# Kernel tuning notes

Hardware: AMD Instinct MI355X
Metric: run time of the kernel (lower is better)

Reference implementation:

```python
import jax, jax.numpy as jnp
import numpy as np

NUM_DIM = 2
N, P, Q, C = 2048, 2048, 64, 2

def _mlp(x, layers, activate_final):
    n = len(layers)
    for i, (w, b) in enumerate(layers):
        x = x @ w + b
        if i < n - 1 or activate_final:
            x = jnp.tanh(x)
    return x

def setup_inputs() -> dict:
    key = jax.random.key(0)
    ks = jax.random.split(key, 24)
    s = 0.3  # param scale for numerical sanity
    return {
        "phase_coords": jax.random.normal(ks[0], (N, 2 * NUM_DIM), jnp.float32),
        "boundary_coords": jax.random.normal(ks[1], (N, 2 * NUM_DIM), jnp.float32),
        "coeff_position": jax.random.normal(ks[2], (P, NUM_DIM), jnp.float32),
        "coeff_values": jax.random.uniform(ks[3], (P, C), jnp.float32),
        "scattering_kernel_coords": jax.random.normal(ks[4], (Q, NUM_DIM), jnp.float32),
        "scattering_kernel": jax.random.uniform(ks[5], (Q,), jnp.float32),
        "velocity_weights": jax.random.uniform(ks[6], (Q,), jnp.float32) / Q,
        "attn_w1": s * jax.random.normal(ks[7], (6, 32), jnp.float32),
        "attn_b1": jnp.zeros((32,), jnp.float32),
        "attn_w2": s * jax.random.normal(ks[8], (32, 32), jnp.float32),
        "attn_b2": jnp.zeros((32,), jnp.float32),
        "attn_w3": s * jax.random.normal(ks[9], (32, 1), jnp.float32),
        "attn_b3": jnp.zeros((1,), jnp.float32),
        "green_w1": s * jax.random.normal(ks[10], (4 * NUM_DIM + C, 64), jnp.float32),
        "green_b1": jnp.zeros((64,), jnp.float32),
        "green_w2": s * jax.random.normal(ks[11], (64, 64), jnp.float32),
        "green_b2": jnp.zeros((64,), jnp.float32),
        "green_w3": s * jax.random.normal(ks[12], (64, 64), jnp.float32),
        "green_b3": jnp.zeros((64,), jnp.float32),
        "res_w": s * jax.random.normal(ks[13], (64, 64), jnp.float32),
        "res_b": jnp.zeros((64,), jnp.float32),
        "final_w": s * jax.random.normal(ks[14], (64, 1), jnp.float32),
        "final_b": jnp.zeros((1,), jnp.float32),
    }

def reference(phase_coords, boundary_coords, coeff_position, coeff_values,
              scattering_kernel_coords, scattering_kernel, velocity_weights,
              attn_w1, attn_b1, attn_w2, attn_b2, attn_w3, attn_b3,
              green_w1, green_b1, green_w2, green_b2, green_w3, green_b3,
              res_w, res_b, final_w, final_b):
    attn_layers = [(attn_w1, attn_b1), (attn_w2, attn_b2), (attn_w3, attn_b3)]
    green_layers = [(green_w1, green_b1), (green_w2, green_b2), (green_w3, green_b3)]

    x, v = phase_coords[:, :NUM_DIM], phase_coords[:, NUM_DIM:]     # (N,2),(N,2)
    xp, vp = boundary_coords[:, :NUM_DIM], boundary_coords[:, NUM_DIM:]

    # --- CoefficientNet: MLP attention logits + geometric mask + softmax over P ---
    ang = v / jnp.sqrt(jnp.sum(v**2, -1, keepdims=True) + 1e-16)     # (N,2)
    rel = x[:, None, :] - coeff_position[None, :, :]                 # (N,P,2)
    dist = jnp.sqrt(jnp.sum(rel**2, -1) + 1e-16)                     # (N,P)
    pos_loc = jnp.einsum('npd,nd->np', rel, ang)                     # (N,P)
    ang_loc = pos_loc / (dist + 1e-8)
    frames = jnp.stack([ang_loc, pos_loc], -1)                       # (N,P,2)
    coords = jnp.concatenate([x, v], -1)                             # (N,4)
    qk = jnp.concatenate(
        [jnp.broadcast_to(coords[:, None, :], (coords.shape[0], frames.shape[1], coords.shape[1])), frames], -1)  # (N,P,6)
    logits = _mlp(qk, attn_layers, False)[..., 0]                    # (N,P)
    logits = jnp.where(pos_loc > 0, logits, -1e30)
    aw = jax.nn.softmax(logits, axis=-1)
    coeff = jnp.exp(-(aw @ coeff_values))                            # (N,C)

    # --- GreenFunctionBlock (coefficients only depend on (x,v)) ---
    g0 = jnp.exp(_mlp(jnp.concatenate([x, v, xp, vp, coeff], -1), green_layers, True))  # (N,64)

    # --- res block depth=1: quadrature over velocity_prime (argnum=3) ---
    w_quad = (1.0 - scattering_kernel) * velocity_weights            # (Q,)
    Nn = x.shape[0]; Qq = scattering_kernel_coords.shape[0]
    base = jnp.concatenate([x, v, xp], -1)                           # (N,6)
    inp_q = jnp.concatenate([
        jnp.broadcast_to(base[:, None, :], (Nn, Qq, base.shape[1])),
        jnp.broadcast_to(scattering_kernel_coords[None, :, :], (Nn, Qq, NUM_DIM)),
        jnp.broadcast_to(coeff[:, None, :], (Nn, Qq, coeff.shape[1])),
    ], -1)                                                           # (N,Q,10)
    gq = jnp.exp(_mlp(inp_q, green_layers, True))                    # (N,Q,64)
    quad = jnp.einsum('nqh,q->nh', gq, w_quad)                       # (N,64)
    res = jnp.tanh(quad @ res_w + res_b)                             # widths[-1:], activate_final
    out = g0 + res
    return out @ final_w + final_b                                   # (N,1)
```

## Files before the change

kernel.cpp:

```cpp
#include <hip/hip_runtime.h>

#define NN 2048
#define PP 2048
#define QQ 64
#define GR_ROWS 4
#define GR_SLOTS 80
#define GR_MT 5

typedef __attribute__((ext_vector_type(8))) short short8;
typedef __attribute__((ext_vector_type(4))) float f32x4;
typedef __attribute__((ext_vector_type(4))) unsigned u32x4;

union V4 { u32x4 u; short8 s; };

#if __has_builtin(__builtin_amdgcn_exp2f)
#define EXP2(x) __builtin_amdgcn_exp2f(x)
#else
#define EXP2(x) exp2f(x)
#endif

__device__ __forceinline__ float fast_rcp(float x) { return __builtin_amdgcn_rcpf(x); }

__device__ __forceinline__ float fast_tanh(float x) {
    float t = EXP2(x * 2.885390082f);
    return 1.0f - 2.0f * __builtin_amdgcn_rcpf(t + 1.0f);
}

__device__ __forceinline__ unsigned cvt_pk_bf16(float lo, float hi) {
    unsigned r;
    asm("v_cvt_pk_bf16_f32 %0, %1, %2" : "=v"(r) : "v"(lo), "v"(hi));
    return r;
}
__device__ __forceinline__ unsigned short bf16_bits(float f) {
    unsigned u = __builtin_bit_cast(unsigned, f);
    u += 0x7FFFu + ((u >> 16) & 1u);
    return (unsigned short)(u >> 16);
}

__global__ __launch_bounds__(512) void attn_kernel(
    const float* __restrict__ pc, const float* __restrict__ cp,
    const float* __restrict__ cv,
    const float* __restrict__ w1, const float* __restrict__ b1,
    const float* __restrict__ w2, const float* __restrict__ b2,
    const float* __restrict__ w3, const float* __restrict__ b3,
    float* __restrict__ coeff_out)
{
    __shared__ float2 sap[8][272];
    __shared__ unsigned short sidx[8][272];
    __shared__ float sred[24];

    const int t = threadIdx.x;
    const int w = t >> 6, lane = t & 63;
    const int c15 = lane & 15, kg = lane >> 4;
    const int k0 = kg * 8;
    const int n  = blockIdx.x;
    const int p0 = w * 256;

    const float b3v = b3[0];
    const float x0 = pc[n*4+0], x1 = pc[n*4+1];
    const float v0 = pc[n*4+2], v1 = pc[n*4+3];
    const float rinv = __builtin_amdgcn_rsqf(v0*v0 + v1*v1 + 1e-16f);
    const float a0 = v0 * rinv, a1 = v1 * rinv;

    int cnt = 0;
    #pragma unroll
    for (int i = 0; i < 4; ++i) {
        const int p = p0 + i*64 + lane;
        const float2 cpp = ((const float2*)cp)[p];
        const float r0 = x0 - cpp.x;
        const float r1 = x1 - cpp.y;
        const float pos = fmaf(r0, a0, r1*a1);
        const bool f = pos > 0.0f;
        const unsigned long long mask = __ballot(f);
        if (f) {
            const int idx = cnt + __popcll(mask & ((1ull << lane) - 1ull));
            const float dist = sqrtf(r0*r0 + r1*r1 + 1e-16f);
            const float angl = pos * fast_rcp(dist + 1e-8f);
            sap[w][idx]  = make_float2(angl, pos);
            sidx[w][idx] = (unsigned short)p;
        }
        cnt += __popcll(mask);
    }
    if (lane < 16) {
        sap[w][cnt + lane]  = make_float2(0.0f, 0.0f);
        sidx[w][cnt + lane] = 0;
    }

    union BF { short8 s8; unsigned u[4]; } B0, B1;
    #pragma unroll
    for (int j2 = 0; j2 < 4; ++j2) {
        const int ka = k0 + 2*j2, kb = ka + 1;
        B0.u[j2] = cvt_pk_bf16(w2[ka*32 + c15],      w2[kb*32 + c15]);
        B1.u[j2] = cvt_pk_bf16(w2[ka*32 + c15 + 16], w2[kb*32 + c15 + 16]);
    }
    float b2a[4], b2b[4], w3a[4], w3b[4];
    #pragma unroll
    for (int r = 0; r < 4; ++r) {
        b2a[r] = b2[kg*4 + r];      b2b[r] = b2[16 + kg*4 + r];
        w3a[r] = w3[kg*4 + r];      w3b[r] = w3[16 + kg*4 + r];
    }
    float cfrag[8], w1a[8], w1b[8];
    #pragma unroll
    for (int j = 0; j < 8; ++j) {
        const int k = k0 + j;
        float c = b1[k];
        c = fmaf(x0, w1[0*32+k], c);
        c = fmaf(x1, w1[1*32+k], c);
        c = fmaf(v0, w1[2*32+k], c);
        c = fmaf(v1, w1[3*32+k], c);
        cfrag[j] = c;
        w1a[j] = w1[4*32+k];
        w1b[j] = w1[5*32+k];
    }
    float sw3 = 0.0f;
    #pragma unroll
    for (int j = 0; j < 32; ++j) sw3 += fabsf(w3[j]);
    const float Lb = fabsf(b3v) + sw3;
    const float C_E = (b3v - Lb) * 1.44269504f;

    float s = 0.0f, q0 = 0.0f, q1 = 0.0f;
    const int nt = (cnt + 15) >> 4;
    #pragma unroll 2
    for (int tile = 0; tile < nt; ++tile) {
        const int li = tile*16 + c15;
        const float2 ap = sap[w][li];
        const float angl = ap.x, pos = ap.y;

        float pre[8], h[8];
        #pragma unroll
        for (int j = 0; j < 8; ++j)
            pre[j] = fmaf(angl, w1a[j], fmaf(pos, w1b[j], cfrag[j]));
        #pragma unroll
        for (int j = 0; j < 8; ++j) h[j] = fast_tanh(pre[j]);

        union AF { short8 s8; unsigned u[4]; } H;
        #pragma unroll
        for (int j2 = 0; j2 < 4; ++j2)
            H.u[j2] = cvt_pk_bf16(h[2*j2], h[2*j2+1]);

        f32x4 acca = {b2a[0], b2a[1], b2a[2], b2a[3]};
        f32x4 accb = {b2b[0], b2b[1], b2b[2], b2b[3]};
        acca = __builtin_amdgcn_mfma_f32_16x16x32_bf16(B0.s8, H.s8, acca, 0, 0, 0);
        accb = __builtin_amdgcn_mfma_f32_16x16x32_bf16(B1.s8, H.s8, accb, 0, 0, 0);

        float lg = 0.0f;
        #pragma unroll
        for (int r = 0; r < 4; ++r) {
            lg = fmaf(fast_tanh(acca[r]), w3a[r], lg);
            lg = fmaf(fast_tanh(accb[r]), w3b[r], lg);
        }
        lg += __shfl_xor(lg, 16);
        lg += __shfl_xor(lg, 32);

        const bool val = (kg == 0) && (li < cnt);
        const int pidx = (int)sidx[w][li];
        const float2 cvv = ((const float2*)cv)[pidx];
        const float e = val ? EXP2(fmaf(lg, 1.44269504f, C_E)) : 0.0f;
        s += e;
        q0 = fmaf(e, cvv.x, q0);
        q1 = fmaf(e, cvv.y, q1);
    }

    #pragma unroll
    for (int off = 1; off < 64; off <<= 1) {
        s  += __shfl_xor(s, off);
        q0 += __shfl_xor(q0, off);
        q1 += __shfl_xor(q1, off);
    }
    if (lane == 0) {
        sred[w*3 + 0] = s;
        sred[w*3 + 1] = q0;
        sred[w*3 + 2] = q1;
    }
    __syncthreads();
    if (t == 0) {
        float S = 0.0f, Q0 = 0.0f, Q1 = 0.0f;
        #pragma unroll
        for (int i = 0; i < 8; ++i) {
            S  += sred[i*3 + 0];
            Q0 += sred[i*3 + 1];
            Q1 += sred[i*3 + 2];
        }
        if (!(S > 0.0f)) {
            S = (float)PP; Q0 = 0.0f; Q1 = 0.0f;
            for (int p = 0; p < PP; ++p) { Q0 += cv[2*p]; Q1 += cv[2*p+1]; }
        }
        const float invS = fast_rcp(S);
        coeff_out[n*2+0] = __expf(-Q0 * invS);
        coeff_out[n*2+1] = __expf(-Q1 * invS);
    }
}

__global__ __launch_bounds__(256) void green_kernel(
    const float* __restrict__ pc,  const float* __restrict__ bc,
    const float* __restrict__ skc, const float* __restrict__ sk,
    const float* __restrict__ vw,
    const float* __restrict__ gw1, const float* __restrict__ gb1,
    const float* __restrict__ gw2, const float* __restrict__ gb2,
    const float* __restrict__ gw3, const float* __restrict__ gb3,
    const float* __restrict__ rw,  const float* __restrict__ rb,
    const float* __restrict__ fw,  const float* __restrict__ fb,
    const float* __restrict__ coeff,
    float* __restrict__ out)
{
    __shared__ unsigned short sinA[GR_ROWS*GR_SLOTS*16];
    __shared__ unsigned short shb[4][16*64];
    __shared__ float swq[GR_SLOTS];
    __shared__ float sg0[4][64];
    __shared__ float squad[4][64];

    const int t = threadIdx.x;
    const int w = t >> 6, lane = t & 63;
    const int c15 = lane & 15, kg = lane >> 4;
    const int n0 = blockIdx.x * GR_ROWS;

    V4 Bw1[4], Bw2[2][4], Bw3[2][4];
    #pragma unroll
    for (int nt = 0; nt < 4; ++nt) {
        const int col = c15 + nt*16;
        #pragma unroll
        for (int j2 = 0; j2 < 4; ++j2) {
            const int ka = kg*8 + 2*j2, kb = ka + 1;
            const float va = (ka < 10) ? gw1[ka*64 + col] : 0.0f;
            const float vb = (kb < 10) ? gw1[kb*64 + col] : 0.0f;
            Bw1[nt].u[j2] = cvt_pk_bf16(va, vb);
        }
        #pragma unroll
        for (int kt = 0; kt < 2; ++kt) {
            #pragma unroll
            for (int j2 = 0; j2 < 4; ++j2) {
                const int ka = kt*32 + kg*8 + 2*j2, kb = ka + 1;
                Bw2[kt][nt].u[j2] = cvt_pk_bf16(gw2[ka*64 + col], gw2[kb*64 + col]);
                Bw3[kt][nt].u[j2] = cvt_pk_bf16(gw3[ka*64 + col], gw3[kb*64 + col]);
            }
        }
    }
    float b1c[4], b2c[4], b3c[4];
    #pragma unroll
    for (int nt = 0; nt < 4; ++nt) {
        b1c[nt] = gb1[c15 + nt*16];
        b2c[nt] = gb2[c15 + nt*16];
        b3c[nt] = gb3[c15 + nt*16];
    }

    for (int row = t; row < GR_ROWS*GR_SLOTS; row += 256) {
        const int nl = row / GR_SLOTS;
        const int s  = row - nl*GR_SLOTS;
        const int n  = n0 + nl;
        u32x4 lo = {0u,0u,0u,0u}, hi = {0u,0u,0u,0u};
        if (s <= 64) {
            const float X0 = pc[n*4+0], X1 = pc[n*4+1];
            const float V0 = pc[n*4+2], V1 = pc[n*4+3];
            const float XP0 = bc[n*4+0], XP1 = bc[n*4+1];
            float I6, I7;
            if (s == 64) { I6 = bc[n*4+2]; I7 = bc[n*4+3]; }
            else         { I6 = skc[s*2+0]; I7 = skc[s*2+1]; }
            const float C0 = coeff[n*2+0], C1 = coeff[n*2+1];
            lo[0] = cvt_pk_bf16(X0, X1);
            lo[1] = cvt_pk_bf16(V0, V1);
            lo[2] = cvt_pk_bf16(XP0, XP1);
            lo[3] = cvt_pk_bf16(I6, I7);
            hi[0] = cvt_pk_bf16(C0, C1);
        }
        ((u32x4*)sinA)[row*2 + 0] = lo;
        ((u32x4*)sinA)[row*2 + 1] = hi;
    }
    if (t < GR_SLOTS)
        swq[t] = (t < QQ) ? (1.0f - sk[t]) * vw[t] : 0.0f;
    __syncthreads();

    unsigned short* hb = &shb[w][0];
    float qacc[4] = {0.f, 0.f, 0.f, 0.f};

    #pragma unroll 1
    for (int T = 0; T < GR_MT; ++T) {
        const int rm = w*GR_SLOTS + T*16 + c15;
        V4 A1; A1.u = (u32x4){0u,0u,0u,0u};
        if (kg < 2) A1.u = ((u32x4*)sinA)[rm*2 + kg];

        f32x4 acc1[4];
        #pragma unroll
        for (int nt = 0; nt < 4; ++nt) {
            f32x4 a = {b1c[nt], b1c[nt], b1c[nt], b1c[nt]};
            acc1[nt] = __builtin_amdgcn_mfma_f32_16x16x32_bf16(A1.s, Bw1[nt].s, a, 0, 0, 0);
        }
        #pragma unroll
        for (int nt = 0; nt < 4; ++nt) {
            #pragma unroll
            for (int r = 0; r < 4; ++r) {
                const int rl = kg*4 + r;
                hb[rl*64 + ((c15 + nt*16) ^ ((rl&7)<<3))] = bf16_bits(fast_tanh(acc1[nt][r]));
            }
        }
        V4 A2[2];
        #pragma unroll
        for (int kt = 0; kt < 2; ++kt)
            A2[kt].u = ((u32x4*)hb)[(c15*64 + ((kt*32 + kg*8) ^ ((c15&7)<<3))) >> 3];
        f32x4 acc2[4];
        #pragma unroll
        for (int nt = 0; nt < 4; ++nt) {
            f32x4 a = {b2c[nt], b2c[nt], b2c[nt], b2c[nt]};
            a = __builtin_amdgcn_mfma_f32_16x16x32_bf16(A2[0].s, Bw2[0][nt].s, a, 0, 0, 0);
            acc2[nt] = __builtin_amdgcn_mfma_f32_16x16x32_bf16(A2[1].s, Bw2[1][nt].s, a, 0, 0, 0);
        }
        #pragma unroll
        for (int nt = 0; nt < 4; ++nt) {
            #pragma unroll
            for (int r = 0; r < 4; ++r) {
                const int rl = kg*4 + r;
                hb[rl*64 + ((c15 + nt*16) ^ ((rl&7)<<3))] = bf16_bits(fast_tanh(acc2[nt][r]));
            }
        }
        V4 A3[2];
        #pragma unroll
        for (int kt = 0; kt < 2; ++kt)
            A3[kt].u = ((u32x4*)hb)[(c15*64 + ((kt*32 + kg*8) ^ ((c15&7)<<3))) >> 3];
        f32x4 acc3[4];
        #pragma unroll
        for (int nt = 0; nt < 4; ++nt) {
            f32x4 a = {b3c[nt], b3c[nt], b3c[nt], b3c[nt]};
            a = __builtin_amdgcn_mfma_f32_16x16x32_bf16(A3[0].s, Bw3[0][nt].s, a, 0, 0, 0);
            acc3[nt] = __builtin_amdgcn_mfma_f32_16x16x32_bf16(A3[1].s, Bw3[1][nt].s, a, 0, 0, 0);
        }
        #pragma unroll
        for (int r = 0; r < 4; ++r) {
            const int s = T*16 + kg*4 + r;
            const float wq = swq[s];
            #pragma unroll
            for (int nt = 0; nt < 4; ++nt) {
                const float g = __expf(fast_tanh(acc3[nt][r]));
                qacc[nt] = fmaf(wq, g, qacc[nt]);
                if (T == GR_MT-1 && kg == 0 && r == 0) sg0[w][c15 + nt*16] = g;
            }
        }
    }

    #pragma unroll
    for (int nt = 0; nt < 4; ++nt) {
        qacc[nt] += __shfl_xor(qacc[nt], 16);
        qacc[nt] += __shfl_xor(qacc[nt], 32);
    }
    if (kg == 0) {
        #pragma unroll
        for (int nt = 0; nt < 4; ++nt) squad[w][c15 + nt*16] = qacc[nt];
    }

    const int k = lane;
    float r0a = rb[k], r1a = 0.f, r2a = 0.f, r3a = 0.f;
    #pragma unroll
    for (int j = 0; j < 64; j += 4) {
        const float4 qd = *(const float4*)&squad[w][j];
        r0a = fmaf(qd.x, rw[(j+0)*64 + k], r0a);
        r1a = fmaf(qd.y, rw[(j+1)*64 + k], r1a);
        r2a = fmaf(qd.z, rw[(j+2)*64 + k], r2a);
        r3a = fmaf(qd.w, rw[(j+3)*64 + k], r3a);
    }
    const float resv = fast_tanh((r0a + r1a) + (r2a + r3a));
    float term = (sg0[w][k] + resv) * fw[k];
    #pragma unroll
    for (int off = 32; off; off >>= 1) term += __shfl_xor(term, off);
    if (lane == 0) out[n0 + w] = term + fb[0];
}

extern "C" void kernel_launch(void* const* d_in, const int* in_sizes, int n_in,
                              void* d_out, int out_size, void* d_ws, size_t ws_size,
                              hipStream_t stream) {
    const float* pc  = (const float*)d_in[0];
    const float* bc  = (const float*)d_in[1];
    const float* cp  = (const float*)d_in[2];
    const float* cv  = (const float*)d_in[3];
    const float* skc = (const float*)d_in[4];
    const float* sk  = (const float*)d_in[5];
    const float* vw  = (const float*)d_in[6];
    const float* aw1 = (const float*)d_in[7];
    const float* ab1 = (const float*)d_in[8];
    const float* aw2 = (const float*)d_in[9];
    const float* ab2 = (const float*)d_in[10];
    const float* aw3 = (const float*)d_in[11];
    const float* ab3 = (const float*)d_in[12];
    const float* gw1 = (const float*)d_in[13];
    const float* gb1 = (const float*)d_in[14];
    const float* gw2 = (const float*)d_in[15];
    const float* gb2 = (const float*)d_in[16];
    const float* gw3 = (const float*)d_in[17];
    const float* gb3 = (const float*)d_in[18];
    const float* rw  = (const float*)d_in[19];
    const float* rb  = (const float*)d_in[20];
    const float* fw  = (const float*)d_in[21];
    const float* fb  = (const float*)d_in[22];

    float* coeff = (float*)d_ws;
    float* outp  = (float*)d_out;

    attn_kernel<<<NN, 512, 0, stream>>>(pc, cp, cv, aw1, ab1, aw2, ab2, aw3, ab3, coeff);
    green_kernel<<<NN/GR_ROWS, 256, 0, stream>>>(pc, bc, skc, sk, vw,
                                                 gw1, gb1, gw2, gb2, gw3, gb3,
                                                 rw, rb, fw, fb, coeff, outp);
}
```

Before: 80.24 us.

## Process two query rows per attention block and pack angle/pos as bf16 in LDS

The attention kernel now handles two query points per 512-thread block, with four waves per point each scanning 512 candidates instead of eight waves each scanning 256. This halves the block count and the per-block fixed costs such as weight loading and the final reduction. The stored angle/position pair is packed into one bf16x2 word to fit the larger per-wave LDS buffers. That rounds the MLP inputs earlier than before and may slightly change accuracy. Fewer waves cooperate per point, so load imbalance across waves may grow.

```diff
diff --git a/kernel.cpp b/kernel.cpp
--- a/kernel.cpp
+++ b/kernel.cpp
@@ -35,6 +35,12 @@
     unsigned u = __builtin_bit_cast(unsigned, f);
     u += 0x7FFFu + ((u >> 16) & 1u);
     return (unsigned short)(u >> 16);
+}
+__device__ __forceinline__ float bf16_lo(unsigned pk) {
+    return __builtin_bit_cast(float, pk << 16);
+}
+__device__ __forceinline__ float bf16_hi(unsigned pk) {
+    return __builtin_bit_cast(float, pk & 0xFFFF0000u);
 }
 
 __global__ __launch_bounds__(512) void attn_kernel(
@@ -45,16 +51,16 @@
     const float* __restrict__ w3, const float* __restrict__ b3,
     float* __restrict__ coeff_out)
 {
-    __shared__ float2 sap[8][272];
-    __shared__ unsigned short sidx[8][272];
+    __shared__ unsigned sap[8][528];
+    __shared__ unsigned short sidx[8][528];
     __shared__ float sred[24];
 
     const int t = threadIdx.x;
     const int w = t >> 6, lane = t & 63;
     const int c15 = lane & 15, kg = lane >> 4;
     const int k0 = kg * 8;
-    const int n  = blockIdx.x;
-    const int p0 = w * 256;
+    const int n  = blockIdx.x * 2 + (w >> 2);
+    const int p0 = (w & 3) * 512;
 
     const float b3v = b3[0];
     const float x0 = pc[n*4+0], x1 = pc[n*4+1];
@@ -64,7 +70,7 @@
 
     int cnt = 0;
     #pragma unroll
-    for (int i = 0; i < 4; ++i) {
+    for (int i = 0; i < 8; ++i) {
         const int p = p0 + i*64 + lane;
         const float2 cpp = ((const float2*)cp)[p];
         const float r0 = x0 - cpp.x;
@@ -76,13 +82,13 @@
             const int idx = cnt + __popcll(mask & ((1ull << lane) - 1ull));
             const float dist = sqrtf(r0*r0 + r1*r1 + 1e-16f);
             const float angl = pos * fast_rcp(dist + 1e-8f);
-            sap[w][idx]  = make_float2(angl, pos);
+            sap[w][idx]  = cvt_pk_bf16(angl, pos);
             sidx[w][idx] = (unsigned short)p;
         }
         cnt += __popcll(mask);
     }
     if (lane < 16) {
-        sap[w][cnt + lane]  = make_float2(0.0f, 0.0f);
+        sap[w][cnt + lane]  = 0u;
         sidx[w][cnt + lane] = 0;
     }
 
@@ -123,8 +129,8 @@
     #pragma unroll 2
     for (int tile = 0; tile < nt; ++tile) {
         const int li = tile*16 + c15;
-        const float2 ap = sap[w][li];
-        const float angl = ap.x, pos = ap.y;
+        const unsigned pk = sap[w][li];
+        const float angl = bf16_lo(pk), pos = bf16_hi(pk);
 
         float pre[8], h[8];
         #pragma unroll
@@ -173,13 +179,13 @@
         sred[w*3 + 2] = q1;
     }
     __syncthreads();
-    if (t == 0) {
+    if (lane == 0 && (w == 0 || w == 4)) {
         float S = 0.0f, Q0 = 0.0f, Q1 = 0.0f;
         #pragma unroll
-        for (int i = 0; i < 8; ++i) {
-            S  += sred[i*3 + 0];
-            Q0 += sred[i*3 + 1];
-            Q1 += sred[i*3 + 2];
+        for (int i = 0; i < 4; ++i) {
+            S  += sred[(w + i)*3 + 0];
+            Q0 += sred[(w + i)*3 + 1];
+            Q1 += sred[(w + i)*3 + 2];
         }
         if (!(S > 0.0f)) {
             S = (float)PP; Q0 = 0.0f; Q1 = 0.0f;
@@ -392,7 +398,7 @@
     float* coeff = (float*)d_ws;
     float* outp  = (float*)d_out;
 
-    attn_kernel<<<NN, 512, 0, stream>>>(pc, cp, cv, aw1, ab1, aw2, ab2, aw3, ab3, coeff);
+    attn_kernel<<<NN/2, 512, 0, stream>>>(pc, cp, cv, aw1, ab1, aw2, ab2, aw3, ab3, coeff);
     green_kernel<<<NN/GR_ROWS, 256, 0, stream>>>(pc, bc, skc, sk, vw,
                                                  gw1, gb1, gw2, gb2, gw3, gb3,
                                                  rw, rb, fw, fb, coeff, outp);
```

Measured after the change: 83.35 us. 3.9% more time.

## Fuse attention and Green-function kernels into one per-row kernel

Applied to the files above, without the earlier changes.

Merges the attention-coefficient kernel and the Green-function MLP/quadrature kernel into a single 512-thread kernel, one block per row. Coefficients pass through shared memory instead of a global workspace, which removes the second launch and the global round trip. The 80 quadrature slots are split across 5 waves, and a final wave does the residual layer and output. The cost is that each block reloads and converts the Green MLP weights to bf16 for a single row instead of amortising them over 4 rows. Three of the eight waves also sit idle during the Green phase, and shared-memory use per block rises.

```diff
diff --git a/kernel.cpp b/kernel.cpp
--- a/kernel.cpp
+++ b/kernel.cpp
@@ -3,9 +3,6 @@
 #define NN 2048
 #define PP 2048
 #define QQ 64
-#define GR_ROWS 4
-#define GR_SLOTS 80
-#define GR_MT 5
 
 typedef __attribute__((ext_vector_type(8))) short short8;
 typedef __attribute__((ext_vector_type(4))) float f32x4;
@@ -37,17 +34,31 @@
     return (unsigned short)(u >> 16);
 }
 
-__global__ __launch_bounds__(512) void attn_kernel(
-    const float* __restrict__ pc, const float* __restrict__ cp,
-    const float* __restrict__ cv,
+__global__ __launch_bounds__(512) void fused_kernel(
+    const float* __restrict__ pc,  const float* __restrict__ bc,
+    const float* __restrict__ cp,  const float* __restrict__ cv,
+    const float* __restrict__ skc, const float* __restrict__ sk,
+    const float* __restrict__ vw,
     const float* __restrict__ w1, const float* __restrict__ b1,
     const float* __restrict__ w2, const float* __restrict__ b2,
     const float* __restrict__ w3, const float* __restrict__ b3,
-    float* __restrict__ coeff_out)
+    const float* __restrict__ gw1, const float* __restrict__ gb1,
+    const float* __restrict__ gw2, const float* __restrict__ gb2,
+    const float* __restrict__ gw3, const float* __restrict__ gb3,
+    const float* __restrict__ rw,  const float* __restrict__ rb,
+    const float* __restrict__ fw,  const float* __restrict__ fb,
+    float* __restrict__ out)
 {
     __shared__ float2 sap[8][272];
     __shared__ unsigned short sidx[8][272];
     __shared__ float sred[24];
+    __shared__ float scoef[2];
+    __shared__ unsigned short sinA[80*16];
+    __shared__ unsigned short shb[5][16*64];
+    __shared__ float swq[80];
+    __shared__ float sq[5][64];
+    __shared__ float sg0[64];
+    __shared__ float squadL[64];
 
     const int t = threadIdx.x;
     const int w = t >> 6, lane = t & 63;
@@ -119,9 +130,9 @@
     const float C_E = (b3v - Lb) * 1.44269504f;
 
     float s = 0.0f, q0 = 0.0f, q1 = 0.0f;
-    const int nt = (cnt + 15) >> 4;
+    const int ntl = (cnt + 15) >> 4;
     #pragma unroll 2
-    for (int tile = 0; tile < nt; ++tile) {
+    for (int tile = 0; tile < ntl; ++tile) {
         const int li = tile*16 + c15;
         const float2 ap = sap[w][li];
         const float angl = ap.x, pos = ap.y;
@@ -173,6 +184,7 @@
         sred[w*3 + 2] = q1;
     }
     __syncthreads();
+
     if (t == 0) {
         float S = 0.0f, Q0 = 0.0f, Q1 = 0.0f;
         #pragma unroll
@@ -186,180 +198,149 @@
             for (int p = 0; p < PP; ++p) { Q0 += cv[2*p]; Q1 += cv[2*p+1]; }
         }
         const float invS = fast_rcp(S);
-        coeff_out[n*2+0] = __expf(-Q0 * invS);
-        coeff_out[n*2+1] = __expf(-Q1 * invS);
-    }
-}
-
-__global__ __launch_bounds__(256) void green_kernel(
-    const float* __restrict__ pc,  const float* __restrict__ bc,
-    const float* __restrict__ skc, const float* __restrict__ sk,
-    const float* __restrict__ vw,
-    const float* __restrict__ gw1, const float* __restrict__ gb1,
-    const float* __restrict__ gw2, const float* __restrict__ gb2,
-    const float* __restrict__ gw3, const float* __restrict__ gb3,
-    const float* __restrict__ rw,  const float* __restrict__ rb,
-    const float* __restrict__ fw,  const float* __restrict__ fb,
-    const float* __restrict__ coeff,
-    float* __restrict__ out)
-{
-    __shared__ unsigned short sinA[GR_ROWS*GR_SLOTS*16];
-    __shared__ unsigned short shb[4][16*64];
-    __shared__ float swq[GR_SLOTS];
-    __shared__ float sg0[4][64];
-    __shared__ float squad[4][64];
-
-    const int t = threadIdx.x;
-    const int w = t >> 6, lane = t & 63;
-    const int c15 = lane & 15, kg = lane >> 4;
-    const int n0 = blockIdx.x * GR_ROWS;
-
-    V4 Bw1[4], Bw2[2][4], Bw3[2][4];
-    #pragma unroll
-    for (int nt = 0; nt < 4; ++nt) {
-        const int col = c15 + nt*16;
-        #pragma unroll
-        for (int j2 = 0; j2 < 4; ++j2) {
-            const int ka = kg*8 + 2*j2, kb = ka + 1;
-            const float va = (ka < 10) ? gw1[ka*64 + col] : 0.0f;
-            const float vb = (kb < 10) ? gw1[kb*64 + col] : 0.0f;
-            Bw1[nt].u[j2] = cvt_pk_bf16(va, vb);
-        }
-        #pragma unroll
-        for (int kt = 0; kt < 2; ++kt) {
-            #pragma unroll
-            for (int j2 = 0; j2 < 4; ++j2) {
-                const int ka = kt*32 + kg*8 + 2*j2, kb = ka + 1;
-                Bw2[kt][nt].u[j2] = cvt_pk_bf16(gw2[ka*64 + col], gw2[kb*64 + col]);
-                Bw3[kt][nt].u[j2] = cvt_pk_bf16(gw3[ka*64 + col], gw3[kb*64 + col]);
-            }
-        }
-    }
-    float b1c[4], b2c[4], b3c[4];
-    #pragma unroll
-    for (int nt = 0; nt < 4; ++nt) {
-        b1c[nt] = gb1[c15 + nt*16];
-        b2c[nt] = gb2[c15 + nt*16];
-        b3c[nt] = gb3[c15 + nt*16];
-    }
-
-    for (int row = t; row < GR_ROWS*GR_SLOTS; row += 256) {
-        const int nl = row / GR_SLOTS;
-        const int s  = row - nl*GR_SLOTS;
-        const int n  = n0 + nl;
+        scoef[0] = __expf(-Q0 * invS);
+        scoef[1] = __expf(-Q1 * invS);
+    }
+    __syncthreads();
+
+    if (t < 80) {
+        const int slot = t;
         u32x4 lo = {0u,0u,0u,0u}, hi = {0u,0u,0u,0u};
-        if (s <= 64) {
-            const float X0 = pc[n*4+0], X1 = pc[n*4+1];
-            const float V0 = pc[n*4+2], V1 = pc[n*4+3];
+        if (slot <= 64) {
             const float XP0 = bc[n*4+0], XP1 = bc[n*4+1];
             float I6, I7;
-            if (s == 64) { I6 = bc[n*4+2]; I7 = bc[n*4+3]; }
-            else         { I6 = skc[s*2+0]; I7 = skc[s*2+1]; }
-            const float C0 = coeff[n*2+0], C1 = coeff[n*2+1];
-            lo[0] = cvt_pk_bf16(X0, X1);
-            lo[1] = cvt_pk_bf16(V0, V1);
+            if (slot == 64) { I6 = bc[n*4+2]; I7 = bc[n*4+3]; }
+            else            { I6 = skc[slot*2+0]; I7 = skc[slot*2+1]; }
+            lo[0] = cvt_pk_bf16(x0, x1);
+            lo[1] = cvt_pk_bf16(v0, v1);
             lo[2] = cvt_pk_bf16(XP0, XP1);
             lo[3] = cvt_pk_bf16(I6, I7);
-            hi[0] = cvt_pk_bf16(C0, C1);
-        }
-        ((u32x4*)sinA)[row*2 + 0] = lo;
-        ((u32x4*)sinA)[row*2 + 1] = hi;
-    }
-    if (t < GR_SLOTS)
-        swq[t] = (t < QQ) ? (1.0f - sk[t]) * vw[t] : 0.0f;
+            hi[0] = cvt_pk_bf16(scoef[0], scoef[1]);
+        }
+        ((u32x4*)sinA)[slot*2 + 0] = lo;
+        ((u32x4*)sinA)[slot*2 + 1] = hi;
+        swq[slot] = (slot < QQ) ? (1.0f - sk[slot]) * vw[slot] : 0.0f;
+    }
     __syncthreads();
 
-    unsigned short* hb = &shb[w][0];
-    float qacc[4] = {0.f, 0.f, 0.f, 0.f};
-
-    #pragma unroll 1
-    for (int T = 0; T < GR_MT; ++T) {
-        const int rm = w*GR_SLOTS + T*16 + c15;
+    if (w < 5) {
+        const int rm = w*16 + c15;
         V4 A1; A1.u = (u32x4){0u,0u,0u,0u};
-        if (kg < 2) A1.u = ((u32x4*)sinA)[rm*2 + kg];
-
-        f32x4 acc1[4];
-        #pragma unroll
-        for (int nt = 0; nt < 4; ++nt) {
-            f32x4 a = {b1c[nt], b1c[nt], b1c[nt], b1c[nt]};
-            acc1[nt] = __builtin_amdgcn_mfma_f32_16x16x32_bf16(A1.s, Bw1[nt].s, a, 0, 0, 0);
+        if (kg < 2) A1.u = ((const u32x4*)sinA)[rm*2 + kg];
+        unsigned short* hb = &shb[w][0];
+
+        f32x4 acc[4];
+        #pragma unroll
+        for (int nt = 0; nt < 4; ++nt) {
+            const int col = c15 + nt*16;
+            V4 B;
+            #pragma unroll
+            for (int j2 = 0; j2 < 4; ++j2) {
+                const int ka = kg*8 + 2*j2, kb = ka + 1;
+                const float va = (ka < 10) ? gw1[ka*64 + col] : 0.0f;
+                const float vb = (kb < 10) ? gw1[kb*64 + col] : 0.0f;
+                B.u[j2] = cvt_pk_bf16(va, vb);
+            }
+            const float bb = gb1[col];
+            f32x4 a = {bb, bb, bb, bb};
+            acc[nt] = __builtin_amdgcn_mfma_f32_16x16x32_bf16(A1.s, B.s, a, 0, 0, 0);
         }
         #pragma unroll
         for (int nt = 0; nt < 4; ++nt) {
             #pragma unroll
             for (int r = 0; r < 4; ++r) {
                 const int rl = kg*4 + r;
-                hb[rl*64 + ((c15 + nt*16) ^ ((rl&7)<<3))] = bf16_bits(fast_tanh(acc1[nt][r]));
+                hb[rl*64 + ((c15 + nt*16) ^ ((rl&7)<<3))] = bf16_bits(fast_tanh(acc[nt][r]));
             }
         }
         V4 A2[2];
         #pragma unroll
         for (int kt = 0; kt < 2; ++kt)
             A2[kt].u = ((u32x4*)hb)[(c15*64 + ((kt*32 + kg*8) ^ ((c15&7)<<3))) >> 3];
-        f32x4 acc2[4];
-        #pragma unroll
-        for (int nt = 0; nt < 4; ++nt) {
-            f32x4 a = {b2c[nt], b2c[nt], b2c[nt], b2c[nt]};
-            a = __builtin_amdgcn_mfma_f32_16x16x32_bf16(A2[0].s, Bw2[0][nt].s, a, 0, 0, 0);
-            acc2[nt] = __builtin_amdgcn_mfma_f32_16x16x32_bf16(A2[1].s, Bw2[1][nt].s, a, 0, 0, 0);
+        #pragma unroll
+        for (int nt = 0; nt < 4; ++nt) {
+            const int col = c15 + nt*16;
+            V4 Ba, Bb;
+            #pragma unroll
+            for (int j2 = 0; j2 < 4; ++j2) {
+                const int ka = kg*8 + 2*j2, kb = ka + 1;
+                Ba.u[j2] = cvt_pk_bf16(gw2[ka*64 + col],        gw2[kb*64 + col]);
+                Bb.u[j2] = cvt_pk_bf16(gw2[(32+ka)*64 + col],   gw2[(32+kb)*64 + col]);
+            }
+            const float bb = gb2[col];
+            f32x4 a = {bb, bb, bb, bb};
+            a = __builtin_amdgcn_mfma_f32_16x16x32_bf16(A2[0].s, Ba.s, a, 0, 0, 0);
+            acc[nt] = __builtin_amdgcn_mfma_f32_16x16x32_bf16(A2[1].s, Bb.s, a, 0, 0, 0);
         }
         #pragma unroll
         for (int nt = 0; nt < 4; ++nt) {
             #pragma unroll
             for (int r = 0; r < 4; ++r) {
                 const int rl = kg*4 + r;
-                hb[rl*64 + ((c15 + nt*16) ^ ((rl&7)<<3))] = bf16_bits(fast_tanh(acc2[nt][r]));
+                hb[rl*64 + ((c15 + nt*16) ^ ((rl&7)<<3))] = bf16_bits(fast_tanh(acc[nt][r]));
             }
         }
         V4 A3[2];
         #pragma unroll
         for (int kt = 0; kt < 2; ++kt)
             A3[kt].u = ((u32x4*)hb)[(c15*64 + ((kt*32 + kg*8) ^ ((c15&7)<<3))) >> 3];
-        f32x4 acc3[4];
-        #pragma unroll
-        for (int nt = 0; nt < 4; ++nt) {
-            f32x4 a = {b3c[nt], b3c[nt], b3c[nt], b3c[nt]};
-            a = __builtin_amdgcn_mfma_f32_16x16x32_bf16(A3[0].s, Bw3[0][nt].s, a, 0, 0, 0);
-            acc3[nt] = __builtin_amdgcn_mfma_f32_16x16x32_bf16(A3[1].s, Bw3[1][nt].s, a, 0, 0, 0);
-        }
+        #pragma unroll
+        for (int nt = 0; nt < 4; ++nt) {
+            const int col = c15 + nt*16;
+            V4 Ba, Bb;
+            #pragma unroll
+            for (int j2 = 0; j2 < 4; ++j2) {
+                const int ka = kg*8 + 2*j2, kb = ka + 1;
+                Ba.u[j2] = cvt_pk_bf16(gw3[ka*64 + col],        gw3[kb*64 + col]);
+                Bb.u[j2] = cvt_pk_bf16(gw3[(32+ka)*64 + col],   gw3[(32+kb)*64 + col]);
+            }
+            const float bb = gb3[col];
+            f32x4 a = {bb, bb, bb, bb};
+            a = __builtin_amdgcn_mfma_f32_16x16x32_bf16(A3[0].s, Ba.s, a, 0, 0, 0);
+            acc[nt] = __builtin_amdgcn_mfma_f32_16x16x32_bf16(A3[1].s, Bb.s, a, 0, 0, 0);
+        }
+        float qpart[4] = {0.f, 0.f, 0.f, 0.f};
         #pragma unroll
         for (int r = 0; r < 4; ++r) {
-            const int s = T*16 + kg*4 + r;
-            const float wq = swq[s];
+            const int slot = w*16 + kg*4 + r;
+            const float wq = swq[slot];
             #pragma unroll
             for (int nt = 0; nt < 4; ++nt) {
-                const float g = __expf(fast_tanh(acc3[nt][r]));
-                qacc[nt] = fmaf(wq, g, qacc[nt]);
-                if (T == GR_MT-1 && kg == 0 && r == 0) sg0[w][c15 + nt*16] = g;
-            }
-        }
-    }
-
-    #pragma unroll
-    for (int nt = 0; nt < 4; ++nt) {
-        qacc[nt] += __shfl_xor(qacc[nt], 16);
-        qacc[nt] += __shfl_xor(qacc[nt], 32);
-    }
-    if (kg == 0) {
-        #pragma unroll
-        for (int nt = 0; nt < 4; ++nt) squad[w][c15 + nt*16] = qacc[nt];
-    }
-
-    const int k = lane;
-    float r0a = rb[k], r1a = 0.f, r2a = 0.f, r3a = 0.f;
-    #pragma unroll
-    for (int j = 0; j < 64; j += 4) {
-        const float4 qd = *(const float4*)&squad[w][j];
-        r0a = fmaf(qd.x, rw[(j+0)*64 + k], r0a);
-        r1a = fmaf(qd.y, rw[(j+1)*64 + k], r1a);
-        r2a = fmaf(qd.z, rw[(j+2)*64 + k], r2a);
-        r3a = fmaf(qd.w, rw[(j+3)*64 + k], r3a);
-    }
-    const float resv = fast_tanh((r0a + r1a) + (r2a + r3a));
-    float term = (sg0[w][k] + resv) * fw[k];
-    #pragma unroll
-    for (int off = 32; off; off >>= 1) term += __shfl_xor(term, off);
-    if (lane == 0) out[n0 + w] = term + fb[0];
+                const float g = __expf(fast_tanh(acc[nt][r]));
+                qpart[nt] = fmaf(wq, g, qpart[nt]);
+                if (w == 4 && kg == 0 && r == 0) sg0[c15 + nt*16] = g;
+            }
+        }
+        #pragma unroll
+        for (int nt = 0; nt < 4; ++nt) {
+            qpart[nt] += __shfl_xor(qpart[nt], 16);
+            qpart[nt] += __shfl_xor(qpart[nt], 32);
+        }
+        if (kg == 0) {
+            #pragma unroll
+            for (int nt = 0; nt < 4; ++nt) sq[w][c15 + nt*16] = qpart[nt];
+        }
+    }
+    __syncthreads();
+
+    if (w == 0) {
+        const int k = lane;
+        squadL[k] = sq[0][k] + sq[1][k] + sq[2][k] + sq[3][k] + sq[4][k];
+        float r0a = rb[k], r1a = 0.f, r2a = 0.f, r3a = 0.f;
+        #pragma unroll
+        for (int j = 0; j < 64; j += 4) {
+            const float4 qd = *(const float4*)&squadL[j];
+            r0a = fmaf(qd.x, rw[(j+0)*64 + k], r0a);
+            r1a = fmaf(qd.y, rw[(j+1)*64 + k], r1a);
+            r2a = fmaf(qd.z, rw[(j+2)*64 + k], r2a);
+            r3a = fmaf(qd.w, rw[(j+3)*64 + k], r3a);
+        }
+        const float resv = fast_tanh((r0a + r1a) + (r2a + r3a));
+        float term = (sg0[k] + resv) * fw[k];
+        #pragma unroll
+        for (int off = 32; off; off >>= 1) term += __shfl_xor(term, off);
+        if (k == 0) out[n] = term + fb[0];
+    }
 }
 
 extern "C" void kernel_launch(void* const* d_in, const int* in_sizes, int n_in,
@@ -389,11 +370,10 @@
     const float* fw  = (const float*)d_in[21];
     const float* fb  = (const float*)d_in[22];
 
-    float* coeff = (float*)d_ws;
-    float* outp  = (float*)d_out;
-
-    attn_kernel<<<NN, 512, 0, stream>>>(pc, cp, cv, aw1, ab1, aw2, ab2, aw3, ab3, coeff);
-    green_kernel<<<NN/GR_ROWS, 256, 0, stream>>>(pc, bc, skc, sk, vw,
-                                                 gw1, gb1, gw2, gb2, gw3, gb3,
-                                                 rw, rb, fw, fb, coeff, outp);
-}
+    float* outp = (float*)d_out;
+
+    fused_kernel<<<NN, 512, 0, stream>>>(pc, bc, cp, cv, skc, sk, vw,
+                                         aw1, ab1, aw2, ab2, aw3, ab3,
+                                         gw1, gb1, gw2, gb2, gw3, gb3,
+                                         rw, rb, fw, fb, outp);
+}
```

After: 91.75 us. +14.3%, slower.
